# Kernel optimization log

Hardware: AMD Instinct MI355X
Metric: run time of the kernel (lower is better)

The kernel has to match this reference:

```python
import jax, jax.numpy as jnp
import numpy as np

B, N = 4, 32768
IN_CH, OUT_CH, SD = 4, 4, 3
WIDTH, DEPTH, M, H, FFN = 256, 8, 32, 8, 1024
CF, TF, FB = 8, 4, 1000
IN_DIM = IN_CH + 2 * CF + 2 * TF  # 28
DH = WIDTH // H


def setup_inputs() -> dict:
    key = jax.random.key(0)
    ks = jax.random.split(key, 16)
    r = lambda i, shape, s=0.02: jax.random.normal(ks[i], shape, dtype=jnp.float32) * s
    return {
        "features": jax.random.normal(ks[0], (B, N, IN_CH), dtype=jnp.float32),
        "coords": jax.random.uniform(ks[1], (B, N, SD), minval=-1.0, maxval=1.0),
        "t_norm": jax.random.uniform(ks[2], (B,)),
        "freq_matrix": jax.random.normal(ks[3], (SD, CF), dtype=jnp.float32),
        "omega": FB ** (-jnp.arange(TF, dtype=jnp.float32) / TF),
        "in_w": r(4, (IN_DIM, WIDTH)), "in_b": jnp.zeros((WIDTH,)),
        "ln1_g": jnp.ones((DEPTH, WIDTH)), "ln1_b": jnp.zeros((DEPTH, WIDTH)),
        "slice_w": r(5, (DEPTH, WIDTH, M)), "slice_b": jnp.zeros((DEPTH, M)),
        "qkv_w": r(6, (DEPTH, WIDTH, 3 * WIDTH)), "qkv_b": jnp.zeros((DEPTH, 3 * WIDTH)),
        "attn_out_w": r(7, (DEPTH, WIDTH, WIDTH)), "attn_out_b": jnp.zeros((DEPTH, WIDTH)),
        "ln2_g": jnp.ones((DEPTH, WIDTH)), "ln2_b": jnp.zeros((DEPTH, WIDTH)),
        "ffn1_w": r(8, (DEPTH, WIDTH, FFN)), "ffn1_b": jnp.zeros((DEPTH, FFN)),
        "ffn2_w": r(9, (DEPTH, FFN, WIDTH)), "ffn2_b": jnp.zeros((DEPTH, WIDTH)),
        "out_w": r(10, (WIDTH, OUT_CH)), "out_b": jnp.zeros((OUT_CH,)),
    }


def _ln(x, g, b):
    mu = x.mean(-1, keepdims=True)
    var = ((x - mu) ** 2).mean(-1, keepdims=True)
    return (x - mu) * jax.lax.rsqrt(var + 1e-5) * g + b


def _mha(z, qkv_w, qkv_b, ow, ob):
    # z: (B, M, WIDTH). Standard torch nn.MultiheadAttention self-attn.
    qkv = z @ qkv_w + qkv_b                      # (B, M, 3*WIDTH)
    q, k, v = jnp.split(qkv, 3, axis=-1)
    sh = (z.shape[0], M, H, DH)
    q = q.reshape(sh).transpose(0, 2, 1, 3)      # (B, H, M, DH)
    k = k.reshape(sh).transpose(0, 2, 1, 3)
    v = v.reshape(sh).transpose(0, 2, 1, 3)
    scores = jnp.einsum('bhmd,bhkd->bhmk', q, k) / jnp.sqrt(jnp.float32(DH))
    attn = jax.nn.softmax(scores, axis=-1)
    o = jnp.einsum('bhmk,bhkd->bhmd', attn, v)   # (B, H, M, DH)
    o = o.transpose(0, 2, 1, 3).reshape(z.shape[0], M, WIDTH)
    return o @ ow + ob


def _physics_attention(h, sw, sb, qkv_w, qkv_b, ow, ob):
    # h: (B, N, WIDTH)
    w = jax.nn.softmax(h @ sw + sb, axis=-1)                 # (B, N, M)
    wsum = jnp.clip(w.sum(axis=1), 1e-8, None)               # (B, M)
    slices = jnp.einsum('bnm,bnd->bmd', w, h) / wsum[..., None]
    slices_out = _mha(slices, qkv_w, qkv_b, ow, ob)          # (B, M, WIDTH)
    return jnp.einsum('bnm,bmd->bnd', w, slices_out)         # (B, N, WIDTH)


def _forward(features, coords, t_norm, freq_matrix, omega, in_w, in_b,
             ln1_g, ln1_b, slice_w, slice_b, qkv_w, qkv_b, attn_out_w, attn_out_b,
             ln2_g, ln2_b, ffn1_w, ffn1_b, ffn2_w, ffn2_b, out_w, out_b):
    # Spatial LFF encoding
    proj = 2.0 * jnp.pi * (coords @ freq_matrix)             # (B, N, CF)
    sp = jnp.concatenate([jnp.sin(proj), jnp.cos(proj)], axis=-1)
    # Temporal sinusoidal encoding, broadcast to all nodes
    angles = omega[None, :] * (t_norm * FB)[:, None]         # (B, TF)
    te = jnp.concatenate([jnp.sin(angles), jnp.cos(angles)], axis=-1)
    te = jnp.broadcast_to(te[:, None, :], (features.shape[0], features.shape[1], 2 * TF))
    x = jnp.concatenate([features, sp, te], axis=-1) @ in_w + in_b  # (B, N, WIDTH)
    for i in range(DEPTH):
        h = _ln(x, ln1_g[i], ln1_b[i])
        x = x + _physics_attention(h, slice_w[i], slice_b[i], qkv_w[i], qkv_b[i],
                                   attn_out_w[i], attn_out_b[i])
        h2 = _ln(x, ln2_g[i], ln2_b[i])
        x = x + jax.nn.gelu(h2 @ ffn1_w[i] + ffn1_b[i], approximate=False) @ ffn2_w[i] + ffn2_b[i]
    return x @ out_w + out_b                                 # (B, N, OUT_CH)


def reference(features, coords, t_norm, freq_matrix, omega, in_w, in_b,
              ln1_g, ln1_b, slice_w, slice_b, qkv_w, qkv_b, attn_out_w, attn_out_b,
              ln2_g, ln2_b, ffn1_w, ffn1_b, ffn2_w, ffn2_b, out_w, out_b):
    return _forward(features, coords, t_norm, freq_matrix, omega, in_w, in_b,
                    ln1_g, ln1_b, slice_w, slice_b, qkv_w, qkv_b, attn_out_w, attn_out_b,
                    ln2_g, ln2_b, ffn1_w, ffn1_b, ffn2_w, ffn2_b, out_w, out_b)
```

## Files before the change

kernel.cpp:

```cpp
#include <hip/hip_runtime.h>

#define BB 4
#define NN 32768
#define BN 131072
#define WD 256
#define NDEPTH 8
#define MS 32
#define NH 8
#define DHD 32
#define FF 1024

typedef float f32x4 __attribute__((ext_vector_type(4)));
typedef float f32x2 __attribute__((ext_vector_type(2)));
typedef _Float16 f16x8 __attribute__((ext_vector_type(8)));
typedef _Float16 f16x4 __attribute__((ext_vector_type(4)));

__device__ __forceinline__ float rcp_(float x){ return __builtin_amdgcn_rcpf(x); }
__device__ __forceinline__ float rsq_(float x){ return __builtin_amdgcn_rsqf(x); }

__device__ __forceinline__ float gelu_f(float x){
  float z  = 0.70710678118654752f * x;
  float az = fabsf(z);
  float t  = rcp_(fmaf(0.3275911f, az, 1.0f));
  float p  = fmaf(t, 1.061405429f, -1.453152027f);
  p = fmaf(t, p, 1.421413741f);
  p = fmaf(t, p, -0.284496736f);
  p = fmaf(t, p, 0.254829592f);
  p = p * t;
  float e  = __expf(-az*az);
  float er = 1.0f - p*e;
  er = (z < 0.0f) ? -er : er;
  return 0.5f * x * (1.0f + er);
}

__global__ __launch_bounds__(256) void k_prep_w1t(const float* __restrict__ f1w,
                                                  const float* __restrict__ ln2g,
                                                  _Float16* __restrict__ W1T){
  int id = blockIdx.x*256 + threadIdx.x;
  int k = id & 255; int f = (id >> 8) & 1023; int i = id >> 18;
  W1T[id] = (_Float16)(ln2g[i*256+k] * f1w[(size_t)i*262144 + (size_t)k*1024 + f]);
}
__global__ __launch_bounds__(256) void k_prep_w2t(const float* __restrict__ f2w,
                                                  _Float16* __restrict__ W2T){
  int id = blockIdx.x*256 + threadIdx.x;
  int k = id & 1023; int n = (id >> 10) & 255; int i = id >> 18;
  W2T[id] = (_Float16)(f2w[(size_t)i*262144 + (size_t)k*256 + n]);
}
__global__ __launch_bounds__(256) void k_prep_s1c1(const float* __restrict__ f1w,
                                                   const float* __restrict__ ln2g,
                                                   const float* __restrict__ ln2b,
                                                   const float* __restrict__ f1b,
                                                   float* __restrict__ S1, float* __restrict__ C1){
  int fb = blockIdx.x; int i = blockIdx.y; int t = threadIdx.x;
  int f = fb*256 + t;
  const float* w = f1w + (size_t)i*262144 + f;
  float s = 0.f, c = 0.f;
  for (int k = 0; k < 256; ++k){
    float wv = w[(size_t)k*1024];
    s = fmaf(ln2g[i*256+k], wv, s);
    c = fmaf(ln2b[i*256+k], wv, c);
  }
  S1[i*1024+f] = s;
  C1[i*1024+f] = c + f1b[i*1024+f];
}

__global__ __launch_bounds__(256) void k_encode(const float* __restrict__ feat,
                                                const float* __restrict__ coords,
                                                const float* __restrict__ tn,
                                                const float* __restrict__ fm,
                                                const float* __restrict__ om,
                                                const float* __restrict__ in_w,
                                                const float* __restrict__ in_b,
                                                float* __restrict__ X){
  __shared__ float inw[28*256];
  __shared__ float enc[8][28];
  int t = threadIdx.x;
  for (int i = 0; i < 28; ++i) inw[i*256+t] = in_w[i*256+t];
  float bv = in_b[t];
  int row0 = blockIdx.x * 128;
  __syncthreads();
  for (int it = 0; it < 16; ++it){
    int rbase = row0 + it*8;
    if (t < 224){
      int rr = t / 28, j = t - rr*28;
      int row = rbase + rr; int b = row >> 15;
      float v;
      if (j < 4){
        v = feat[(size_t)row*4 + j];
      } else if (j < 20){
        int fi = (j - 4) & 7;
        const float* cp = coords + (size_t)row*3;
        float pr = 6.2831853071795864f * (cp[0]*fm[fi] + cp[1]*fm[8+fi] + cp[2]*fm[16+fi]);
        v = (j < 12) ? sinf(pr) : cosf(pr);
      } else {
        int fi = (j - 20) & 3;
        float ang = om[fi] * (tn[b] * 1000.0f);
        v = (j < 24) ? sinf(ang) : cosf(ang);
      }
      enc[rr][j] = v;
    }
    __syncthreads();
    for (int rr = 0; rr < 8; ++rr){
      float a = bv;
      #pragma unroll 7
      for (int j = 0; j < 28; ++j) a = fmaf(enc[rr][j], inw[j*256+t], a);
      X[(size_t)(rbase+rr)*256 + t] = a;
    }
    __syncthreads();
  }
}

__global__ __launch_bounds__(256) void k_slice(const float* __restrict__ X,
                                               float* __restrict__ Wb,
                                               float* __restrict__ S,
                                               float* __restrict__ WS,
                                               const float* __restrict__ swp,
                                               const float* __restrict__ sbp,
                                               const float* __restrict__ g1p,
                                               const float* __restrict__ b1p){
  __shared__ float hl[256];
  __shared__ float part[256];
  __shared__ float wl[32];
  __shared__ float red[8];
  int t = threadIdx.x;
  int base = (t >> 5) << 5;
  int m = t & 31;
  float swreg[32];
  #pragma unroll
  for (int j = 0; j < 32; ++j) swreg[j] = swp[(size_t)(base+j)*32 + m];
  float g1 = g1p[t], b1 = b1p[t];
  float sbv = (t < 32) ? sbp[t] : 0.f;
  float acc[32];
  #pragma unroll
  for (int i = 0; i < 32; ++i) acc[i] = 0.f;
  float wacc = 0.f;
  int row0 = blockIdx.x * 128;
  int b = row0 >> 15;
  for (int it = 0; it < 128; ++it){
    int row = row0 + it;
    float xv = X[(size_t)row*256 + t];
    float s = xv, q = xv*xv;
    #pragma unroll
    for (int off = 32; off; off >>= 1){ s += __shfl_xor(s, off); q += __shfl_xor(q, off); }
    if ((t & 63) == 0){ red[(t>>6)*2] = s; red[(t>>6)*2+1] = q; }
    __syncthreads();
    float sum = red[0]+red[2]+red[4]+red[6];
    float sq  = red[1]+red[3]+red[5]+red[7];
    float mu  = sum * (1.f/256.f);
    float var = sq * (1.f/256.f) - mu*mu;
    float rstd = rsq_(var + 1e-5f);
    float h = (xv - mu)*rstd*g1 + b1;
    hl[t] = h;
    __syncthreads();
    {
      float p = 0.f;
      #pragma unroll
      for (int j = 0; j < 32; ++j) p = fmaf(hl[base+j], swreg[j], p);
      part[t] = p;
    }
    __syncthreads();
    if (t < 32){
      float lg = sbv;
      #pragma unroll
      for (int g = 0; g < 8; ++g) lg += part[g*32 + t];
      float mx = lg;
      #pragma unroll
      for (int off = 16; off; off >>= 1) mx = fmaxf(mx, __shfl_xor(mx, off));
      float e = __expf(lg - mx);
      float se = e;
      #pragma unroll
      for (int off = 16; off; off >>= 1) se += __shfl_xor(se, off);
      float wv = e * rcp_(se);
      wl[t] = wv;
      Wb[(size_t)row*32 + t] = wv;
      wacc += wv;
    }
    __syncthreads();
    #pragma unroll
    for (int i = 0; i < 32; ++i) acc[i] = fmaf(wl[i], h, acc[i]);
  }
  #pragma unroll 8
  for (int i = 0; i < 32; ++i) atomicAdd(&S[(size_t)(b*32+i)*256 + t], acc[i]);
  if (t < 32) atomicAdd(&WS[b*32 + t], wacc);
}

__global__ __launch_bounds__(256) void k_mha(const float* __restrict__ S,
                                             const float* __restrict__ WS,
                                             float* __restrict__ O,
                                             const float* __restrict__ qkvw,
                                             const float* __restrict__ qkvb){
  __shared__ float zl[32*256];
  __shared__ float qkl[3][32][33];
  __shared__ float att[32][33];
  __shared__ float wsl[32];
  int t = threadIdx.x;
  int b = blockIdx.x >> 3, h = blockIdx.x & 7;
  if (t < 32) wsl[t] = rcp_(fmaxf(WS[b*32+t], 1e-8f));
  __syncthreads();
  for (int i = 0; i < 32; ++i){
    int e = i*256 + t; int mm = e >> 8; int d = e & 255;
    zl[e] = S[(size_t)(b*32+mm)*256 + d] * wsl[mm];
  }
  __syncthreads();
  for (int i = 0; i < 12; ++i){
    int o = i*256 + t;
    int which = o >> 10, rem = o & 1023, mm = rem >> 5, dh = rem & 31;
    int col = which*256 + h*32 + dh;
    float a = qkvb[col];
    const float* zp = &zl[mm*256];
    const float* wp = qkvw + col;
    #pragma unroll 4
    for (int d = 0; d < 256; ++d) a = fmaf(zp[d], wp[(size_t)d*768], a);
    qkl[which][mm][dh] = a;
  }
  __syncthreads();
  for (int i = 0; i < 4; ++i){
    int e = i*256 + t; int mm = e >> 5; int k2 = e & 31;
    float a = 0.f;
    #pragma unroll 8
    for (int d = 0; d < 32; ++d) a = fmaf(qkl[0][mm][d], qkl[1][k2][d], a);
    att[mm][k2] = a * 0.17677669529663687f;
  }
  __syncthreads();
  {
    int mm = t >> 3, j = t & 7;
    float v0 = att[mm][j], v1 = att[mm][j+8], v2 = att[mm][j+16], v3 = att[mm][j+24];
    float mx = fmaxf(fmaxf(v0, v1), fmaxf(v2, v3));
    #pragma unroll
    for (int off = 4; off; off >>= 1) mx = fmaxf(mx, __shfl_xor(mx, off));
    v0 = __expf(v0-mx); v1 = __expf(v1-mx); v2 = __expf(v2-mx); v3 = __expf(v3-mx);
    float sm = v0+v1+v2+v3;
    #pragma unroll
    for (int off = 4; off; off >>= 1) sm += __shfl_xor(sm, off);
    float inv = rcp_(sm);
    att[mm][j] = v0*inv; att[mm][j+8] = v1*inv; att[mm][j+16] = v2*inv; att[mm][j+24] = v3*inv;
  }
  __syncthreads();
  for (int i = 0; i < 4; ++i){
    int e = i*256 + t; int mm = e >> 5; int dh = e & 31;
    float a = 0.f;
    #pragma unroll 8
    for (int k2 = 0; k2 < 32; ++k2) a = fmaf(att[mm][k2], qkl[2][k2][dh], a);
    O[(size_t)(b*32+mm)*256 + h*32 + dh] = a;
  }
}

__global__ __launch_bounds__(256) void k_outproj(const float* __restrict__ O,
                                                 float* __restrict__ SO,
                                                 const float* __restrict__ aow,
                                                 const float* __restrict__ aob){
  __shared__ float orow[256];
  int t = threadIdx.x; int row = blockIdx.x;
  orow[t] = O[(size_t)row*256 + t];
  __syncthreads();
  float a = aob[t];
  #pragma unroll 4
  for (int d = 0; d < 256; ++d) a = fmaf(orow[d], aow[(size_t)d*256 + t], a);
  SO[(size_t)row*256 + t] = a;
}

__global__ __launch_bounds__(256) void k_deslice(float* __restrict__ X,
                                                 const float* __restrict__ Wb,
                                                 const float* __restrict__ SO,
                                                 float* __restrict__ ST){
  __shared__ float wrow[32];
  __shared__ float red[8];
  int t = threadIdx.x;
  int row0 = blockIdx.x * 32;
  int b = row0 >> 15;
  float soc[32];
  #pragma unroll 8
  for (int i = 0; i < 32; ++i) soc[i] = SO[(size_t)(b*32+i)*256 + t];
  for (int it = 0; it < 32; ++it){
    int row = row0 + it;
    if (t < 32) wrow[t] = Wb[(size_t)row*32 + t];
    __syncthreads();
    float xv = X[(size_t)row*256 + t];
    float dv = 0.f;
    #pragma unroll
    for (int i = 0; i < 32; ++i) dv = fmaf(wrow[i], soc[i], dv);
    float xn = xv + dv;
    X[(size_t)row*256 + t] = xn;
    float s = xn, q = xn*xn;
    #pragma unroll
    for (int off = 32; off; off >>= 1){ s += __shfl_xor(s, off); q += __shfl_xor(q, off); }
    if ((t & 63) == 0){ red[(t>>6)*2] = s; red[(t>>6)*2+1] = q; }
    __syncthreads();
    if (t == 0){
      float sum = red[0]+red[2]+red[4]+red[6];
      float sq  = red[1]+red[3]+red[5]+red[7];
      float mu  = sum * (1.f/256.f);
      float var = sq * (1.f/256.f) - mu*mu;
      float rstd = rsq_(var + 1e-5f);
      ST[(size_t)row*2]   = rstd;
      ST[(size_t)row*2+1] = rstd*mu;
    }
    __syncthreads();
  }
}

__global__ __launch_bounds__(256) void k_ffn1(const float* __restrict__ X,
                                              const _Float16* __restrict__ W1T,
                                              const float* __restrict__ S1,
                                              const float* __restrict__ C1,
                                              const float* __restrict__ ST,
                                              _Float16* __restrict__ U, int c0){
  __shared__ _Float16 As[128*40];
  __shared__ _Float16 Bs[128*40];
  __shared__ f32x2 stl[128];
  int t = threadIdx.x;
  int nb = blockIdx.x;
  int my = blockIdx.y;
  int row0 = c0 + my*128;
  int w = t >> 6, l = t & 63;
  int wm = w >> 1, wn = w & 1, lr = l & 15, lk = l >> 4;
  f32x4 acc[4][4] = {};
  for (int ks = 0; ks < 8; ++ks){
    int k0 = ks*32;
    {
      int r = t >> 3, qd = t & 7;
      #pragma unroll
      for (int i = 0; i < 4; ++i){
        int rr = i*32 + r;
        f32x4 v = *reinterpret_cast<const f32x4*>(X + (size_t)(row0+rr)*256 + k0 + qd*4);
        f16x4 hv; hv[0]=(_Float16)v[0]; hv[1]=(_Float16)v[1]; hv[2]=(_Float16)v[2]; hv[3]=(_Float16)v[3];
        *reinterpret_cast<f16x4*>(&As[rr*40 + qd*4]) = hv;
      }
      #pragma unroll
      for (int i = 0; i < 2; ++i){
        int e = i*256 + t; int fr = e >> 2; int qb = e & 3;
        f16x8 hv = *reinterpret_cast<const f16x8*>(W1T + (size_t)(nb*128+fr)*256 + k0 + qb*8);
        *reinterpret_cast<f16x8*>(&Bs[fr*40 + qb*8]) = hv;
      }
    }
    __syncthreads();
    f16x8 a[4], bf[4];
    #pragma unroll
    for (int i = 0; i < 4; ++i) a[i]  = *reinterpret_cast<const f16x8*>(&As[(64*wm + 16*i + lr)*40 + lk*8]);
    #pragma unroll
    for (int i = 0; i < 4; ++i) bf[i] = *reinterpret_cast<const f16x8*>(&Bs[(64*wn + 16*i + lr)*40 + lk*8]);
    #pragma unroll
    for (int mt = 0; mt < 4; ++mt)
      #pragma unroll
      for (int nt = 0; nt < 4; ++nt)
        acc[mt][nt] = __builtin_amdgcn_mfma_f32_16x16x32_f16(a[mt], bf[nt], acc[mt][nt], 0, 0, 0);
    __syncthreads();
  }
  if (t < 128) stl[t] = *reinterpret_cast<const f32x2*>(ST + (size_t)(row0+t)*2);
  __syncthreads();
  #pragma unroll
  for (int nt = 0; nt < 4; ++nt){
    int f = nb*128 + 64*wn + 16*nt + lr;
    float s1 = S1[f], c1 = C1[f];
    #pragma unroll
    for (int mt = 0; mt < 4; ++mt){
      int lrow0 = 64*wm + 16*mt + lk*4;
      #pragma unroll
      for (int e = 0; e < 4; ++e){
        f32x2 st2 = stl[lrow0 + e];
        float u = st2[0]*acc[mt][nt][e] - st2[1]*s1 + c1;
        U[(size_t)(my*128 + lrow0 + e)*1024 + f] = (_Float16)gelu_f(u);
      }
    }
  }
}

__global__ __launch_bounds__(256) void k_ffn2(const _Float16* __restrict__ U,
                                              const _Float16* __restrict__ W2T,
                                              const float* __restrict__ f2b,
                                              float* __restrict__ X, int c0){
  __shared__ _Float16 As[128*40];
  __shared__ _Float16 Bs[128*40];
  int t = threadIdx.x;
  int nb = blockIdx.x;
  int my = blockIdx.y;
  int w = t >> 6, l = t & 63;
  int wm = w >> 1, wn = w & 1, lr = l & 15, lk = l >> 4;
  f32x4 acc[4][4] = {};
  for (int ks = 0; ks < 32; ++ks){
    int k0 = ks*32;
    #pragma unroll
    for (int i = 0; i < 2; ++i){
      int e = i*256 + t; int r = e >> 2; int qb = e & 3;
      f16x8 hv  = *reinterpret_cast<const f16x8*>(U   + (size_t)(my*128+r)*1024 + k0 + qb*8);
      *reinterpret_cast<f16x8*>(&As[r*40 + qb*8]) = hv;
      f16x8 hv2 = *reinterpret_cast<const f16x8*>(W2T + (size_t)(nb*128+r)*1024 + k0 + qb*8);
      *reinterpret_cast<f16x8*>(&Bs[r*40 + qb*8]) = hv2;
    }
    __syncthreads();
    f16x8 a[4], bf[4];
    #pragma unroll
    for (int i = 0; i < 4; ++i) a[i]  = *reinterpret_cast<const f16x8*>(&As[(64*wm + 16*i + lr)*40 + lk*8]);
    #pragma unroll
    for (int i = 0; i < 4; ++i) bf[i] = *reinterpret_cast<const f16x8*>(&Bs[(64*wn + 16*i + lr)*40 + lk*8]);
    #pragma unroll
    for (int mt = 0; mt < 4; ++mt)
      #pragma unroll
      for (int nt = 0; nt < 4; ++nt)
        acc[mt][nt] = __builtin_amdgcn_mfma_f32_16x16x32_f16(a[mt], bf[nt], acc[mt][nt], 0, 0, 0);
    __syncthreads();
  }
  #pragma unroll
  for (int nt = 0; nt < 4; ++nt){
    int c = nb*128 + 64*wn + 16*nt + lr;
    float bv = f2b[c];
    #pragma unroll
    for (int mt = 0; mt < 4; ++mt){
      int gr = c0 + my*128 + 64*wm + 16*mt + lk*4;
      #pragma unroll
      for (int e = 0; e < 4; ++e){
        size_t idx = (size_t)(gr+e)*256 + c;
        X[idx] = X[idx] + acc[mt][nt][e] + bv;
      }
    }
  }
}

__global__ __launch_bounds__(256) void k_final(const float* __restrict__ X,
                                               const float* __restrict__ out_w,
                                               const float* __restrict__ out_b,
                                               float* __restrict__ out){
  int t = threadIdx.x; int w = t >> 6; int l = t & 63;
  f32x4 ow[4];
  #pragma unroll
  for (int j = 0; j < 4; ++j) ow[j] = *reinterpret_cast<const f32x4*>(out_w + (4*l+j)*4);
  f32x4 ob = *reinterpret_cast<const f32x4*>(out_b);
  int row0 = blockIdx.x * 256;
  for (int it = 0; it < 64; ++it){
    int row = row0 + it*4 + w;
    f32x4 xv = *reinterpret_cast<const f32x4*>(X + (size_t)row*256 + 4*l);
    f32x4 p = ow[0]*xv[0];
    p += ow[1]*xv[1]; p += ow[2]*xv[2]; p += ow[3]*xv[3];
    #pragma unroll
    for (int off = 32; off; off >>= 1){
      p[0] += __shfl_xor(p[0], off);
      p[1] += __shfl_xor(p[1], off);
      p[2] += __shfl_xor(p[2], off);
      p[3] += __shfl_xor(p[3], off);
    }
    if (l == 0) *reinterpret_cast<f32x4*>(out + (size_t)row*4) = p + ob;
  }
}

static constexpr size_t OFF_X   = 0;
static constexpr size_t SZ_X    = (size_t)BN*256*4;
static constexpr size_t OFF_W   = OFF_X + SZ_X;
static constexpr size_t SZ_W    = (size_t)BN*32*4;
static constexpr size_t OFF_ST  = OFF_W + SZ_W;
static constexpr size_t SZ_ST   = (size_t)BN*2*4;
static constexpr size_t OFF_S   = OFF_ST + SZ_ST;
static constexpr size_t SZ_S    = (size_t)4*32*256*4;
static constexpr size_t OFF_WS  = OFF_S + SZ_S;
static constexpr size_t OFF_O   = OFF_WS + 1024;
static constexpr size_t OFF_SO  = OFF_O + 131072;
static constexpr size_t OFF_W1T = OFF_SO + 131072;
static constexpr size_t SZ_W1T  = (size_t)8*1024*256*2;
static constexpr size_t OFF_W2T = OFF_W1T + SZ_W1T;
static constexpr size_t OFF_S1  = OFF_W2T + SZ_W1T;
static constexpr size_t OFF_C1  = OFF_S1 + 8*1024*4;
static constexpr size_t OFF_U   = OFF_C1 + 8*1024*4;

extern "C" void kernel_launch(void* const* d_in, const int* in_sizes, int n_in,
                              void* d_out, int out_size, void* d_ws, size_t ws_size,
                              hipStream_t stream) {
  (void)in_sizes; (void)n_in; (void)out_size;
  const float* features = (const float*)d_in[0];
  const float* coords   = (const float*)d_in[1];
  const float* t_norm   = (const float*)d_in[2];
  const float* freqm    = (const float*)d_in[3];
  const float* omega    = (const float*)d_in[4];
  const float* in_w     = (const float*)d_in[5];
  const float* in_b     = (const float*)d_in[6];
  const float* ln1_g    = (const float*)d_in[7];
  const float* ln1_b    = (const float*)d_in[8];
  const float* slice_w  = (const float*)d_in[9];
  const float* slice_b  = (const float*)d_in[10];
  const float* qkv_w    = (const float*)d_in[11];
  const float* qkv_b    = (const float*)d_in[12];
  const float* aow      = (const float*)d_in[13];
  const float* aob      = (const float*)d_in[14];
  const float* ln2_g    = (const float*)d_in[15];
  const float* ln2_b    = (const float*)d_in[16];
  const float* f1w      = (const float*)d_in[17];
  const float* f1b      = (const float*)d_in[18];
  const float* f2w      = (const float*)d_in[19];
  const float* f2b      = (const float*)d_in[20];
  const float* out_w    = (const float*)d_in[21];
  const float* out_b    = (const float*)d_in[22];

  char* ws = (char*)d_ws;
  float*     X   = (float*)(ws + OFF_X);
  float*     Wb  = (float*)(ws + OFF_W);
  float*     ST  = (float*)(ws + OFF_ST);
  float*     S   = (float*)(ws + OFF_S);
  float*     WS  = (float*)(ws + OFF_WS);
  float*     O   = (float*)(ws + OFF_O);
  float*     SO  = (float*)(ws + OFF_SO);
  _Float16*  W1T = (_Float16*)(ws + OFF_W1T);
  _Float16*  W2T = (_Float16*)(ws + OFF_W2T);
  float*     S1  = (float*)(ws + OFF_S1);
  float*     C1  = (float*)(ws + OFF_C1);
  _Float16*  U   = (_Float16*)(ws + OFF_U);

  int CH = 1;
  while (CH < 32 && OFF_U + (size_t)(BN/CH)*FF*2 > ws_size) CH <<= 1;
  int crows = BN / CH;

  k_prep_w1t<<<8192, 256, 0, stream>>>(f1w, ln2_g, W1T);
  k_prep_w2t<<<8192, 256, 0, stream>>>(f2w, W2T);
  k_prep_s1c1<<<dim3(4, 8), 256, 0, stream>>>(f1w, ln2_g, ln2_b, f1b, S1, C1);
  k_encode<<<1024, 256, 0, stream>>>(features, coords, t_norm, freqm, omega, in_w, in_b, X);

  for (int L = 0; L < NDEPTH; ++L){
    hipMemsetAsync(ws + OFF_S, 0, SZ_S + 1024, stream);
    k_slice<<<1024, 256, 0, stream>>>(X, Wb, S, WS,
        slice_w + (size_t)L*8192, slice_b + (size_t)L*32,
        ln1_g + (size_t)L*256, ln1_b + (size_t)L*256);
    k_mha<<<32, 256, 0, stream>>>(S, WS, O,
        qkv_w + (size_t)L*196608, qkv_b + (size_t)L*768);
    k_outproj<<<128, 256, 0, stream>>>(O, SO,
        aow + (size_t)L*65536, aob + (size_t)L*256);
    k_deslice<<<4096, 256, 0, stream>>>(X, Wb, SO, ST);
    for (int c = 0; c < CH; ++c){
      int c0 = c * crows;
      k_ffn1<<<dim3(8, crows/128), 256, 0, stream>>>(X,
          W1T + (size_t)L*262144, S1 + (size_t)L*1024, C1 + (size_t)L*1024, ST, U, c0);
      k_ffn2<<<dim3(2, crows/128), 256, 0, stream>>>(U,
          W2T + (size_t)L*262144, f2b + (size_t)L*256, X, c0);
    }
  }
  k_final<<<512, 256, 0, stream>>>(X, out_w, out_b, (float*)d_out);
}
```

Baseline: 8.131 ms.

## Batch four rows per sync in slice/deslice and transpose QKV weights for MHA

The slice and deslice kernels now handle four rows per iteration with 4-row shared buffers, so block-wide barriers are paid once per group of four rows. In slice, 128 threads compute softmax weights for four rows at once, and per-lane weight sums are reduced in shared memory before one atomic per slice. A new prep kernel transposes the QKV weights, letting MHA read them contiguously with float4 dot products and vectorized S loads. This costs an extra 6 MB of workspace and a one-time transpose, and changes the floating-point summation order.

```diff
diff --git a/kernel.cpp b/kernel.cpp
--- a/kernel.cpp
+++ b/kernel.cpp
@@ -62,6 +62,13 @@
   }
   S1[i*1024+f] = s;
   C1[i*1024+f] = c + f1b[i*1024+f];
+}
+__global__ __launch_bounds__(256) void k_prep_qkvt(const float* __restrict__ qkvw,
+                                                   float* __restrict__ qkvwT){
+  int id = blockIdx.x*256 + threadIdx.x;
+  int d = id & 255; int cl = id >> 8;
+  int c = cl % 768; int L = cl / 768;
+  qkvwT[id] = qkvw[(size_t)L*196608 + (size_t)d*768 + c];
 }
 
 __global__ __launch_bounds__(256) void k_encode(const float* __restrict__ feat,
@@ -118,10 +125,10 @@
                                                const float* __restrict__ sbp,
                                                const float* __restrict__ g1p,
                                                const float* __restrict__ b1p){
-  __shared__ float hl[256];
-  __shared__ float part[256];
-  __shared__ float wl[32];
-  __shared__ float red[8];
+  __shared__ float hl[4][256];
+  __shared__ float part[4][256];
+  __shared__ float wl[4][32];
+  __shared__ float red[4][8];
   int t = threadIdx.x;
   int base = (t >> 5) << 5;
   int m = t & 31;
@@ -129,40 +136,56 @@
   #pragma unroll
   for (int j = 0; j < 32; ++j) swreg[j] = swp[(size_t)(base+j)*32 + m];
   float g1 = g1p[t], b1 = b1p[t];
-  float sbv = (t < 32) ? sbp[t] : 0.f;
+  float sbv = sbp[t & 31];
   float acc[32];
   #pragma unroll
   for (int i = 0; i < 32; ++i) acc[i] = 0.f;
   float wacc = 0.f;
   int row0 = blockIdx.x * 128;
   int b = row0 >> 15;
-  for (int it = 0; it < 128; ++it){
-    int row = row0 + it;
-    float xv = X[(size_t)row*256 + t];
-    float s = xv, q = xv*xv;
-    #pragma unroll
-    for (int off = 32; off; off >>= 1){ s += __shfl_xor(s, off); q += __shfl_xor(q, off); }
-    if ((t & 63) == 0){ red[(t>>6)*2] = s; red[(t>>6)*2+1] = q; }
-    __syncthreads();
-    float sum = red[0]+red[2]+red[4]+red[6];
-    float sq  = red[1]+red[3]+red[5]+red[7];
-    float mu  = sum * (1.f/256.f);
-    float var = sq * (1.f/256.f) - mu*mu;
-    float rstd = rsq_(var + 1e-5f);
-    float h = (xv - mu)*rstd*g1 + b1;
-    hl[t] = h;
-    __syncthreads();
-    {
+  int wv_id = t >> 6;
+  for (int it = 0; it < 32; ++it){
+    int rb = row0 + it*4;
+    float xv[4], sm[4], qm[4];
+    #pragma unroll
+    for (int r = 0; r < 4; ++r) xv[r] = X[(size_t)(rb+r)*256 + t];
+    #pragma unroll
+    for (int r = 0; r < 4; ++r){ sm[r] = xv[r]; qm[r] = xv[r]*xv[r]; }
+    #pragma unroll
+    for (int off = 32; off; off >>= 1){
+      #pragma unroll
+      for (int r = 0; r < 4; ++r){ sm[r] += __shfl_xor(sm[r], off); qm[r] += __shfl_xor(qm[r], off); }
+    }
+    if ((t & 63) == 0){
+      #pragma unroll
+      for (int r = 0; r < 4; ++r){ red[r][wv_id*2] = sm[r]; red[r][wv_id*2+1] = qm[r]; }
+    }
+    __syncthreads();
+    float h[4];
+    #pragma unroll
+    for (int r = 0; r < 4; ++r){
+      float sum = red[r][0]+red[r][2]+red[r][4]+red[r][6];
+      float sq  = red[r][1]+red[r][3]+red[r][5]+red[r][7];
+      float mu  = sum * (1.f/256.f);
+      float var = sq * (1.f/256.f) - mu*mu;
+      float rstd = rsq_(var + 1e-5f);
+      h[r] = (xv[r] - mu)*rstd*g1 + b1;
+      hl[r][t] = h[r];
+    }
+    __syncthreads();
+    #pragma unroll
+    for (int r = 0; r < 4; ++r){
       float p = 0.f;
       #pragma unroll
-      for (int j = 0; j < 32; ++j) p = fmaf(hl[base+j], swreg[j], p);
-      part[t] = p;
-    }
-    __syncthreads();
-    if (t < 32){
+      for (int j = 0; j < 32; ++j) p = fmaf(hl[r][base+j], swreg[j], p);
+      part[r][t] = p;
+    }
+    __syncthreads();
+    if (t < 128){
+      int r = t >> 5, mm = t & 31;
       float lg = sbv;
       #pragma unroll
-      for (int g = 0; g < 8; ++g) lg += part[g*32 + t];
+      for (int g = 0; g < 8; ++g) lg += part[r][g*32 + mm];
       float mx = lg;
       #pragma unroll
       for (int off = 16; off; off >>= 1) mx = fmaxf(mx, __shfl_xor(mx, off));
@@ -171,23 +194,30 @@
       #pragma unroll
       for (int off = 16; off; off >>= 1) se += __shfl_xor(se, off);
       float wv = e * rcp_(se);
-      wl[t] = wv;
-      Wb[(size_t)row*32 + t] = wv;
+      wl[r][mm] = wv;
+      Wb[(size_t)(rb+r)*32 + mm] = wv;
       wacc += wv;
     }
     __syncthreads();
     #pragma unroll
-    for (int i = 0; i < 32; ++i) acc[i] = fmaf(wl[i], h, acc[i]);
+    for (int r = 0; r < 4; ++r)
+      #pragma unroll
+      for (int i = 0; i < 32; ++i) acc[i] = fmaf(wl[r][i], h[r], acc[i]);
   }
   #pragma unroll 8
   for (int i = 0; i < 32; ++i) atomicAdd(&S[(size_t)(b*32+i)*256 + t], acc[i]);
-  if (t < 32) atomicAdd(&WS[b*32 + t], wacc);
+  if (t < 128) ((float*)hl)[t] = wacc;
+  __syncthreads();
+  if (t < 32){
+    float* f = (float*)hl;
+    atomicAdd(&WS[b*32 + t], f[t] + f[32+t] + f[64+t] + f[96+t]);
+  }
 }
 
 __global__ __launch_bounds__(256) void k_mha(const float* __restrict__ S,
                                              const float* __restrict__ WS,
                                              float* __restrict__ O,
-                                             const float* __restrict__ qkvw,
+                                             const float* __restrict__ qkvwT,
                                              const float* __restrict__ qkvb){
   __shared__ float zl[32*256];
   __shared__ float qkl[3][32][33];
@@ -197,21 +227,25 @@
   int b = blockIdx.x >> 3, h = blockIdx.x & 7;
   if (t < 32) wsl[t] = rcp_(fmaxf(WS[b*32+t], 1e-8f));
   __syncthreads();
-  for (int i = 0; i < 32; ++i){
-    int e = i*256 + t; int mm = e >> 8; int d = e & 255;
-    zl[e] = S[(size_t)(b*32+mm)*256 + d] * wsl[mm];
+  #pragma unroll
+  for (int i = 0; i < 8; ++i){
+    int idx = i*1024 + t*4;
+    int mm = idx >> 8; int d = idx & 255;
+    f32x4 v = *reinterpret_cast<const f32x4*>(S + (size_t)(b*32+mm)*256 + d);
+    v *= wsl[mm];
+    *reinterpret_cast<f32x4*>(&zl[idx]) = v;
   }
   __syncthreads();
   for (int i = 0; i < 12; ++i){
     int o = i*256 + t;
     int which = o >> 10, rem = o & 1023, mm = rem >> 5, dh = rem & 31;
     int col = which*256 + h*32 + dh;
-    float a = qkvb[col];
-    const float* zp = &zl[mm*256];
-    const float* wp = qkvw + col;
-    #pragma unroll 4
-    for (int d = 0; d < 256; ++d) a = fmaf(zp[d], wp[(size_t)d*768], a);
-    qkl[which][mm][dh] = a;
+    const f32x4* zp = reinterpret_cast<const f32x4*>(&zl[mm*256]);
+    const f32x4* wp = reinterpret_cast<const f32x4*>(qkvwT + (size_t)col*256);
+    f32x4 av = {0.f,0.f,0.f,0.f};
+    #pragma unroll 8
+    for (int d4 = 0; d4 < 64; ++d4) av += zp[d4]*wp[d4];
+    qkl[which][mm][dh] = av[0]+av[1]+av[2]+av[3] + qkvb[col];
   }
   __syncthreads();
   for (int i = 0; i < 4; ++i){
@@ -263,39 +297,50 @@
                                                  const float* __restrict__ Wb,
                                                  const float* __restrict__ SO,
                                                  float* __restrict__ ST){
-  __shared__ float wrow[32];
-  __shared__ float red[8];
+  __shared__ float wrow[4][32];
+  __shared__ float red[4][8];
   int t = threadIdx.x;
   int row0 = blockIdx.x * 32;
   int b = row0 >> 15;
+  int wv_id = t >> 6;
   float soc[32];
   #pragma unroll 8
   for (int i = 0; i < 32; ++i) soc[i] = SO[(size_t)(b*32+i)*256 + t];
-  for (int it = 0; it < 32; ++it){
-    int row = row0 + it;
-    if (t < 32) wrow[t] = Wb[(size_t)row*32 + t];
-    __syncthreads();
-    float xv = X[(size_t)row*256 + t];
-    float dv = 0.f;
-    #pragma unroll
-    for (int i = 0; i < 32; ++i) dv = fmaf(wrow[i], soc[i], dv);
-    float xn = xv + dv;
-    X[(size_t)row*256 + t] = xn;
-    float s = xn, q = xn*xn;
-    #pragma unroll
-    for (int off = 32; off; off >>= 1){ s += __shfl_xor(s, off); q += __shfl_xor(q, off); }
-    if ((t & 63) == 0){ red[(t>>6)*2] = s; red[(t>>6)*2+1] = q; }
-    __syncthreads();
-    if (t == 0){
-      float sum = red[0]+red[2]+red[4]+red[6];
-      float sq  = red[1]+red[3]+red[5]+red[7];
+  for (int it = 0; it < 8; ++it){
+    int rb = row0 + it*4;
+    if (t < 128) wrow[t>>5][t&31] = Wb[(size_t)(rb + (t>>5))*32 + (t&31)];
+    __syncthreads();
+    float xn[4], sm[4], qm[4];
+    #pragma unroll
+    for (int r = 0; r < 4; ++r){
+      float xv = X[(size_t)(rb+r)*256 + t];
+      float dv = 0.f;
+      #pragma unroll
+      for (int i = 0; i < 32; ++i) dv = fmaf(wrow[r][i], soc[i], dv);
+      xn[r] = xv + dv;
+      X[(size_t)(rb+r)*256 + t] = xn[r];
+      sm[r] = xn[r]; qm[r] = xn[r]*xn[r];
+    }
+    #pragma unroll
+    for (int off = 32; off; off >>= 1){
+      #pragma unroll
+      for (int r = 0; r < 4; ++r){ sm[r] += __shfl_xor(sm[r], off); qm[r] += __shfl_xor(qm[r], off); }
+    }
+    if ((t & 63) == 0){
+      #pragma unroll
+      for (int r = 0; r < 4; ++r){ red[r][wv_id*2] = sm[r]; red[r][wv_id*2+1] = qm[r]; }
+    }
+    __syncthreads();
+    if (t < 4){
+      int r = t;
+      float sum = red[r][0]+red[r][2]+red[r][4]+red[r][6];
+      float sq  = red[r][1]+red[r][3]+red[r][5]+red[r][7];
       float mu  = sum * (1.f/256.f);
       float var = sq * (1.f/256.f) - mu*mu;
       float rstd = rsq_(var + 1e-5f);
-      ST[(size_t)row*2]   = rstd;
-      ST[(size_t)row*2+1] = rstd*mu;
-    }
-    __syncthreads();
+      ST[(size_t)(rb+r)*2]   = rstd;
+      ST[(size_t)(rb+r)*2+1] = rstd*mu;
+    }
   }
 }
 
@@ -458,7 +503,9 @@
 static constexpr size_t OFF_W2T = OFF_W1T + SZ_W1T;
 static constexpr size_t OFF_S1  = OFF_W2T + SZ_W1T;
 static constexpr size_t OFF_C1  = OFF_S1 + 8*1024*4;
-static constexpr size_t OFF_U   = OFF_C1 + 8*1024*4;
+static constexpr size_t OFF_QT  = OFF_C1 + 8*1024*4;
+static constexpr size_t SZ_QT   = (size_t)8*768*256*4;
+static constexpr size_t OFF_U   = OFF_QT + SZ_QT;
 
 extern "C" void kernel_launch(void* const* d_in, const int* in_sizes, int n_in,
                               void* d_out, int out_size, void* d_ws, size_t ws_size,
@@ -489,18 +536,19 @@
   const float* out_b    = (const float*)d_in[22];
 
   char* ws = (char*)d_ws;
-  float*     X   = (float*)(ws + OFF_X);
-  float*     Wb  = (float*)(ws + OFF_W);
-  float*     ST  = (float*)(ws + OFF_ST);
-  float*     S   = (float*)(ws + OFF_S);
-  float*     WS  = (float*)(ws + OFF_WS);
-  float*     O   = (float*)(ws + OFF_O);
-  float*     SO  = (float*)(ws + OFF_SO);
-  _Float16*  W1T = (_Float16*)(ws + OFF_W1T);
-  _Float16*  W2T = (_Float16*)(ws + OFF_W2T);
-  float*     S1  = (float*)(ws + OFF_S1);
-  float*     C1  = (float*)(ws + OFF_C1);
-  _Float16*  U   = (_Float16*)(ws + OFF_U);
+  float*     X    = (float*)(ws + OFF_X);
+  float*     Wb   = (float*)(ws + OFF_W);
+  float*     ST   = (float*)(ws + OFF_ST);
+  float*     S    = (float*)(ws + OFF_S);
+  float*     WS   = (float*)(ws + OFF_WS);
+  float*     O    = (float*)(ws + OFF_O);
+  float*     SO   = (float*)(ws + OFF_SO);
+  _Float16*  W1T  = (_Float16*)(ws + OFF_W1T);
+  _Float16*  W2T  = (_Float16*)(ws + OFF_W2T);
+  float*     S1   = (float*)(ws + OFF_S1);
+  float*     C1   = (float*)(ws + OFF_C1);
+  float*     QT   = (float*)(ws + OFF_QT);
+  _Float16*  U    = (_Float16*)(ws + OFF_U);
 
   int CH = 1;
   while (CH < 32 && OFF_U + (size_t)(BN/CH)*FF*2 > ws_size) CH <<= 1;
@@ -509,6 +557,7 @@
   k_prep_w1t<<<8192, 256, 0, stream>>>(f1w, ln2_g, W1T);
   k_prep_w2t<<<8192, 256, 0, stream>>>(f2w, W2T);
   k_prep_s1c1<<<dim3(4, 8), 256, 0, stream>>>(f1w, ln2_g, ln2_b, f1b, S1, C1);
+  k_prep_qkvt<<<6144, 256, 0, stream>>>(qkv_w, QT);
   k_encode<<<1024, 256, 0, stream>>>(features, coords, t_norm, freqm, omega, in_w, in_b, X);
 
   for (int L = 0; L < NDEPTH; ++L){
@@ -517,7 +566,7 @@
         slice_w + (size_t)L*8192, slice_b + (size_t)L*32,
         ln1_g + (size_t)L*256, ln1_b + (size_t)L*256);
     k_mha<<<32, 256, 0, stream>>>(S, WS, O,
-        qkv_w + (size_t)L*196608, qkv_b + (size_t)L*768);
+        QT + (size_t)L*196608, qkv_b + (size_t)L*768);
     k_outproj<<<128, 256, 0, stream>>>(O, SO,
         aow + (size_t)L*65536, aob + (size_t)L*256);
     k_deslice<<<4096, 256, 0, stream>>>(X, Wb, SO, ST);
```

Result: faster. 7.315 ms (-10.0%).
